# Performance work log

Hardware: AMD Instinct MI355X
Metric: run time of the kernel (lower is better)

The kernel has to match this reference:

```python
import jax, jax.numpy as jnp
import numpy as np
from math import atanh

B, T, D_IN, H = 16, 1024, 512, 1024
INIT_A = atanh(0.95)


def setup_inputs() -> dict:
    key = jax.random.key(0)
    k1, k2, k3, k4 = jax.random.split(key, 4)
    x = jax.random.normal(k1, (B, T, D_IN), dtype=jnp.float32)
    h0 = jax.random.normal(k2, (B, H), dtype=jnp.float32)
    # raw_a initialized near atanh(0.95) as in the module, with small jitter
    raw_a = INIT_A + 0.01 * jax.random.normal(k3, (H,), dtype=jnp.float32)
    # xavier-uniform for W_x.weight [H, D_IN]
    limit = float(np.sqrt(6.0 / (D_IN + H)))
    W = jax.random.uniform(k4, (H, D_IN), dtype=jnp.float32, minval=-limit, maxval=limit)
    b = jnp.zeros((H,), dtype=jnp.float32)
    return {"x": x, "h0": h0, "raw_a": raw_a, "W": W, "b": b}


def reference(x, h0, raw_a, W, b):
    # h_t = a * h_{t-1} + W x_t + b, computed via cumprod/cumsum parallel-scan trick
    a = jnp.tanh(raw_a)                                   # [H] (rho is None)
    z = jnp.einsum('btd,hd->bth', x, W) + b               # [B,T,H]
    A = jnp.broadcast_to(a, (x.shape[1], a.shape[0]))     # [T,H]
    p = jnp.cumprod(A, axis=0)[None]                      # [1,T,H], p[t] = a^(t+1)
    v = jnp.cumsum(z / jnp.maximum(p, 1e-12), axis=1)     # [B,T,H]
    h = v * p + p * h0[:, None, :]                        # include initial state
    zero_mask = (jnp.abs(a) < 1e-6)[None, None, :]        # degenerate a ~ 0 channels
    h = jnp.where(zero_mask, z, h)
    return h
```

## Files before the change

### kernel.cpp

```cpp
#include <hip/hip_runtime.h>
#include <cstdint>

#define B_DIM 16
#define T_DIM 1024
#define DK    512
#define H_DIM 1024

#define TCH    128
#define NCH    (T_DIM / TCH)
#define NB     128
#define NSTRIP (H_DIM / NB)
#define NKT    16

typedef __bf16 bf16x8 __attribute__((ext_vector_type(8)));
typedef __bf16 bf16x4 __attribute__((ext_vector_type(4)));
typedef float  f32x4  __attribute__((ext_vector_type(4)));

typedef __attribute__((address_space(1))) unsigned int* as1p;
typedef __attribute__((address_space(3))) unsigned int* as3p;

__device__ __forceinline__ void async_cp16(const void* g, void* l) {
  __builtin_amdgcn_global_load_lds((as1p)(uint64_t)g,
                                   (as3p)(uint32_t)(uint64_t)l, 16, 0, 0);
}

__global__ __launch_bounds__(256) void prep(const float* __restrict__ W,
                                            __bf16* __restrict__ wbT,
                                            const float* __restrict__ raw_a,
                                            float4* __restrict__ meta,
                                            unsigned long long* __restrict__ flags) {
  const int bid = blockIdx.x, tid = threadIdx.x;
  if (bid < 512) {
    const int i = bid * 256 + tid;
    const int h  = i >> 7;
    const int k0 = (i & 127) * 4;
    f32x4 v = ((const f32x4*)W)[i];
    bf16x4 o;
    o.x = (__bf16)v.x; o.y = (__bf16)v.y; o.z = (__bf16)v.z; o.w = (__bf16)v.w;
    *(bf16x4*)(wbT + ((size_t)(k0 >> 3) * H_DIM + h) * 8 + (k0 & 7)) = o;
  } else if (bid < 516) {
    const int h = (bid - 512) * 256 + tid;
    const float a = tanhf(raw_a[h]);
    const float la2 = log2f(fabsf(a));
    meta[h] = make_float4(a, la2, (a < 0.f) ? 1.f : 0.f, (fabsf(a) < 1e-6f) ? 1.f : 0.f);
  } else {
    flags[(bid - 516) * 256 + tid] = 0ULL;
  }
}

__global__ __launch_bounds__(256, 4) void fused_rnn(
    const float* __restrict__ xf,
    const __bf16* __restrict__ wbT,
    const float* __restrict__ bias,
    const float4* __restrict__ meta,
    const float* __restrict__ h0g,
    unsigned long long* __restrict__ flags,
    float* __restrict__ out) {
  __shared__ __align__(16) __bf16 As[2][4][TCH][8];
  __shared__ __align__(16) __bf16 Bs[3][4][NB][8];
  float* const scr = (float*)&As[0][0][0][0];

  const int tid  = threadIdx.x;
  const int wave = tid >> 6;
  const int lane = tid & 63;
  const int q  = lane >> 4;
  const int c  = lane & 15;
  const int rw = wave & 1;
  const int cg = wave >> 1;

  const int bid   = blockIdx.x;
  const int g     = bid & 127;
  const int strip = bid >> 7;
  const int b     = g >> 3;
  const int chunk = g & 7;
  const int t0    = chunk * TCH;
  const int n0    = strip * NB;

  const int t8 = tid >> 3;
  const int ck = tid & 7;

  float bias_j[4];
#pragma unroll
  for (int j = 0; j < 4; ++j) bias_j[j] = bias[n0 + cg * 64 + j * 16 + c];

  const float* const xB = xf + (size_t)(b * T_DIM + t0) * DK;

  f32x4 ar[4];
  auto loadA = [&](int kt) {
#pragma unroll
    for (int it = 0; it < 4; ++it)
      ar[it] = *(const f32x4*)(xB + (size_t)(it * 32 + t8) * DK + kt * 32 + ck * 4);
  };
  auto writeA = [&](int buf) {
#pragma unroll
    for (int it = 0; it < 4; ++it) {
      bf16x4 o;
      o.x = (__bf16)ar[it].x; o.y = (__bf16)ar[it].y;
      o.z = (__bf16)ar[it].z; o.w = (__bf16)ar[it].w;
      *(bf16x4*)(&As[buf][ck >> 1][it * 32 + t8][(ck & 1) * 4]) = o;
    }
  };
  auto stageB = [&](int kt, int buf) {
#pragma unroll
    for (int it = 0; it < 2; ++it) {
      const int s = it * 256 + tid;
      const int kq = s >> 7, col = s & 127;
      async_cp16(wbT + ((size_t)(kt * 4 + kq) * H_DIM + n0 + col) * 8,
                 &Bs[buf][kq][col][0]);
    }
  };

  f32x4 acc[4][4];
#pragma unroll
  for (int i = 0; i < 4; ++i)
#pragma unroll
    for (int j = 0; j < 4; ++j)
      acc[i][j] = (f32x4){bias_j[j], bias_j[j], bias_j[j], bias_j[j]};

  loadA(0);
  stageB(0, 0); stageB(1, 1); stageB(2, 2);
  writeA(0);
  loadA(1);
  writeA(1);
  loadA(2);

  for (int kt = 0; kt < NKT; ++kt) {
    const int bufA = kt & 1, bufB = kt % 3;
    if (kt < NKT - 2) asm volatile("s_waitcnt vmcnt(6)" ::: "memory");
    else              asm volatile("s_waitcnt vmcnt(0)" ::: "memory");
    asm volatile("s_waitcnt lgkmcnt(0)" ::: "memory");
    __builtin_amdgcn_s_barrier();

    bf16x8 af[4], bfr[4];
#pragma unroll
    for (int i = 0; i < 4; ++i)
      af[i] = *(const bf16x8*)(&As[bufA][q][rw * 64 + i * 16 + c][0]);
#pragma unroll
    for (int j = 0; j < 4; ++j)
      bfr[j] = *(const bf16x8*)(&Bs[bufB][q][cg * 64 + j * 16 + c][0]);
#pragma unroll
    for (int i = 0; i < 4; ++i)
#pragma unroll
      for (int j = 0; j < 4; ++j)
        acc[i][j] = __builtin_amdgcn_mfma_f32_16x16x32_bf16(af[i], bfr[j], acc[i][j], 0, 0, 0);
    __builtin_amdgcn_sched_barrier(0);
    __builtin_amdgcn_s_barrier();
    __builtin_amdgcn_sched_barrier(0);
    if (kt + 3 < NKT) stageB(kt + 3, bufB);
    if (kt + 2 < NKT) writeA(bufA);
    if (kt + 3 < NKT) loadA(kt + 3);
  }

  float la2_j[4], a_j[4], ai_j[4], sgn_j[4], h0_j[4];
  bool zm_j[4];
#pragma unroll
  for (int j = 0; j < 4; ++j) {
    const int col = n0 + cg * 64 + j * 16 + c;
    const float4 mt = meta[col];
    a_j[j]   = mt.x;
    la2_j[j] = mt.y;
    ai_j[j]  = 1.f / mt.x;
    sgn_j[j] = (mt.z != 0.f) ? -1.f : 1.f;
    zm_j[j]  = mt.w != 0.f;
    h0_j[j]  = h0g[(size_t)b * H_DIM + col];
  }

  float base_[4][4];
  float icarry[4] = {0.f, 0.f, 0.f, 0.f};
#pragma unroll
  for (int i = 0; i < 4; ++i) {
    const int tp10 = t0 + rw * 64 + i * 16 + q * 4 + 1;
#pragma unroll
    for (int j = 0; j < 4; ++j) {
      float u = __builtin_amdgcn_exp2f(-la2_j[j] * (float)tp10) * sgn_j[j];
      f32x4 wv;
#pragma unroll
      for (int r = 0; r < 4; ++r) {
        const float uu = fminf(u, 1e12f);
        const float inv = (u < 0.f) ? 1e12f : uu;
        wv[r] = acc[i][j][r] * inv;
        u *= ai_j[j];
      }
      const float pr0 = wv[0];
      const float pr1 = pr0 + wv[1];
      const float pr2 = pr1 + wv[2];
      const float pr3 = pr2 + wv[3];
      const float x1 = __shfl_xor(pr3, 16, 64);
      const float x2 = __shfl_xor(pr3, 32, 64);
      const float x3 = __shfl_xor(pr3, 48, 64);
      float sq = 0.f;
      if (q >= 2) sq += x2 + x3;
      if (q & 1) sq += x1;
      const float base = icarry[j] + sq;
      base_[i][j] = base;
      acc[i][j] = (f32x4){base + pr0, base + pr1, base + pr2, base + pr3};
      icarry[j] += pr3 + x1 + x2 + x3;
    }
  }
  if (q == 0) {
#pragma unroll
    for (int j = 0; j < 4; ++j) scr[rw * NB + cg * 64 + j * 16 + c] = icarry[j];
  }
  __syncthreads();

  if (tid < NB) {
    const int col = tid;
    const size_t fb = ((size_t)b * NSTRIP + strip) * NCH * NB;
    const float tot = scr[col] + scr[NB + col];
    atomicExch(&flags[fb + (size_t)chunk * NB + col],
               (1ULL << 32) | (unsigned long long)__float_as_uint(tot));
    float s = 0.f;
    for (int p = 0; p < chunk; ++p) {
      unsigned long long v = atomicAdd(&flags[fb + (size_t)p * NB + col], 0ULL);
      while (!(v >> 32)) {
        __builtin_amdgcn_s_sleep(4);
        v = atomicAdd(&flags[fb + (size_t)p * NB + col], 0ULL);
      }
      s += __uint_as_float((unsigned int)v);
    }
    scr[2 * NB + col] = s;
  }
  __syncthreads();

  float cc_[4];
#pragma unroll
  for (int j = 0; j < 4; ++j) {
    const int colL = cg * 64 + j * 16 + c;
    float s = scr[2 * NB + colL];
    if (rw) s += scr[colL];
    cc_[j] = s + h0_j[j];
  }
#pragma unroll
  for (int i = 0; i < 4; ++i) {
    const int tp10 = t0 + rw * 64 + i * 16 + q * 4 + 1;
#pragma unroll
    for (int j = 0; j < 4; ++j) {
      float pv = __builtin_amdgcn_exp2f(la2_j[j] * (float)tp10) * sgn_j[j];
      const int col = n0 + cg * 64 + j * 16 + c;
#pragma unroll
      for (int r = 0; r < 4; ++r) {
        const int tl = t0 + rw * 64 + i * 16 + q * 4 + r;
        const float hv = pv * (acc[i][j][r] + cc_[j]);
        const float wr = acc[i][j][r] - ((r == 0) ? base_[i][j] : acc[i][j][r - 1]);
        out[(size_t)(b * T_DIM + tl) * H_DIM + col] = zm_j[j] ? wr * 1e-12f : hv;
        pv *= a_j[j];
      }
    }
  }
}

extern "C" void kernel_launch(void* const* d_in, const int* in_sizes, int n_in,
                              void* d_out, int out_size, void* d_ws, size_t ws_size,
                              hipStream_t stream) {
  const float* x     = (const float*)d_in[0];
  const float* h0    = (const float*)d_in[1];
  const float* raw_a = (const float*)d_in[2];
  const float* W     = (const float*)d_in[3];
  const float* bias  = (const float*)d_in[4];
  float* out = (float*)d_out;

  char* ws = (char*)d_ws;
  __bf16* wbT = (__bf16*)(ws);
  float4* meta = (float4*)(ws + 1048576);
  unsigned long long* flags =
      (unsigned long long*)(ws + 1048576 + 16384);

  prep<<<1028, 256, 0, stream>>>(W, wbT, raw_a, meta, flags);
  fused_rnn<<<1024, 256, 0, stream>>>(x, wbT, bias, meta, h0, flags, out);
}
```

Measured before the change: 139.7 us.

## Restructure A staging with swizzled 16B LDS writes and shallower prefetch pipeline

```diff
diff --git a/kernel.cpp b/kernel.cpp
--- a/kernel.cpp
+++ b/kernel.cpp
@@ -76,31 +76,35 @@
   const int t0    = chunk * TCH;
   const int n0    = strip * NB;
 
-  const int t8 = tid >> 3;
-  const int ck = tid & 7;
+  const int arow  = tid >> 1;
+  const int khalf = tid & 1;
 
   float bias_j[4];
 #pragma unroll
   for (int j = 0; j < 4; ++j) bias_j[j] = bias[n0 + cg * 64 + j * 16 + c];
 
-  const float* const xB = xf + (size_t)(b * T_DIM + t0) * DK;
+  const float* const xR = xf + (size_t)(b * T_DIM + t0 + arow) * DK + khalf * 16;
 
   f32x4 ar[4];
   auto loadA = [&](int kt) {
 #pragma unroll
     for (int it = 0; it < 4; ++it)
-      ar[it] = *(const f32x4*)(xB + (size_t)(it * 32 + t8) * DK + kt * 32 + ck * 4);
+      ar[it] = *(const f32x4*)(xR + kt * 32 + it * 4);
   };
   auto writeA = [&](int buf) {
 #pragma unroll
-    for (int it = 0; it < 4; ++it) {
-      bf16x4 o;
-      o.x = (__bf16)ar[it].x; o.y = (__bf16)ar[it].y;
-      o.z = (__bf16)ar[it].z; o.w = (__bf16)ar[it].w;
-      *(bf16x4*)(&As[buf][ck >> 1][it * 32 + t8][(ck & 1) * 4]) = o;
+    for (int o = 0; o < 2; ++o) {
+      const int kq = khalf * 2 + o;
+      bf16x8 t;
+      t[0] = (__bf16)ar[o * 2].x; t[1] = (__bf16)ar[o * 2].y;
+      t[2] = (__bf16)ar[o * 2].z; t[3] = (__bf16)ar[o * 2].w;
+      t[4] = (__bf16)ar[o * 2 + 1].x; t[5] = (__bf16)ar[o * 2 + 1].y;
+      t[6] = (__bf16)ar[o * 2 + 1].z; t[7] = (__bf16)ar[o * 2 + 1].w;
+      *(bf16x8*)(&As[buf][kq][arow ^ kq][0]) = t;
     }
   };
-  auto stageB = [&](int kt, int buf) {
+  auto stageB = [&](int kt) {
+    const int buf = kt % 3;
 #pragma unroll
     for (int it = 0; it < 2; ++it) {
       const int s = it * 256 + tid;
@@ -118,37 +122,41 @@
       acc[i][j] = (f32x4){bias_j[j], bias_j[j], bias_j[j], bias_j[j]};
 
   loadA(0);
-  stageB(0, 0); stageB(1, 1); stageB(2, 2);
+  stageB(0); stageB(1);
   writeA(0);
-  loadA(1);
-  writeA(1);
-  loadA(2);
 
   for (int kt = 0; kt < NKT; ++kt) {
     const int bufA = kt & 1, bufB = kt % 3;
-    if (kt < NKT - 2) asm volatile("s_waitcnt vmcnt(6)" ::: "memory");
-    else              asm volatile("s_waitcnt vmcnt(0)" ::: "memory");
+    asm volatile("s_waitcnt vmcnt(2)" ::: "memory");
     asm volatile("s_waitcnt lgkmcnt(0)" ::: "memory");
+    __builtin_amdgcn_sched_barrier(0);
     __builtin_amdgcn_s_barrier();
-
-    bf16x8 af[4], bfr[4];
+    __builtin_amdgcn_sched_barrier(0);
+    if (kt + 1 < NKT) loadA(kt + 1);
+
+    bf16x8 af[4];
 #pragma unroll
     for (int i = 0; i < 4; ++i)
-      af[i] = *(const bf16x8*)(&As[bufA][q][rw * 64 + i * 16 + c][0]);
-#pragma unroll
-    for (int j = 0; j < 4; ++j)
-      bfr[j] = *(const bf16x8*)(&Bs[bufB][q][cg * 64 + j * 16 + c][0]);
-#pragma unroll
-    for (int i = 0; i < 4; ++i)
-#pragma unroll
-      for (int j = 0; j < 4; ++j)
-        acc[i][j] = __builtin_amdgcn_mfma_f32_16x16x32_bf16(af[i], bfr[j], acc[i][j], 0, 0, 0);
+      af[i] = *(const bf16x8*)(&As[bufA][q][(rw * 64 + i * 16 + c) ^ q][0]);
+    bf16x8 b0 = *(const bf16x8*)(&Bs[bufB][q][cg * 64 + 0 * 16 + c][0]);
+    bf16x8 b1 = *(const bf16x8*)(&Bs[bufB][q][cg * 64 + 1 * 16 + c][0]);
+#pragma unroll
+    for (int i = 0; i < 4; ++i) {
+      acc[i][0] = __builtin_amdgcn_mfma_f32_16x16x32_bf16(af[i], b0, acc[i][0], 0, 0, 0);
+      acc[i][1] = __builtin_amdgcn_mfma_f32_16x16x32_bf16(af[i], b1, acc[i][1], 0, 0, 0);
+    }
+    bf16x8 b2 = *(const bf16x8*)(&Bs[bufB][q][cg * 64 + 2 * 16 + c][0]);
+    bf16x8 b3 = *(const bf16x8*)(&Bs[bufB][q][cg * 64 + 3 * 16 + c][0]);
+#pragma unroll
+    for (int i = 0; i < 4; ++i) {
+      acc[i][2] = __builtin_amdgcn_mfma_f32_16x16x32_bf16(af[i], b2, acc[i][2], 0, 0, 0);
+      acc[i][3] = __builtin_amdgcn_mfma_f32_16x16x32_bf16(af[i], b3, acc[i][3], 0, 0, 0);
+    }
     __builtin_amdgcn_sched_barrier(0);
     __builtin_amdgcn_s_barrier();
     __builtin_amdgcn_sched_barrier(0);
-    if (kt + 3 < NKT) stageB(kt + 3, bufB);
-    if (kt + 2 < NKT) writeA(bufA);
-    if (kt + 3 < NKT) loadA(kt + 3);
+    if (kt + 2 < NKT) stageB(kt + 2);
+    if (kt + 1 < NKT) writeA(bufA ^ 1);
   }
 
   float la2_j[4], a_j[4], ai_j[4], sgn_j[4], h0_j[4];
```

Result: no change. 142.0 us (+1.6%).
